# Optimization experiments

Measured on AMD Instinct MI355X. Metric: run time of the kernel, lower is better.

The kernel has to match this reference:

```python
import jax, jax.numpy as jnp
import numpy as np

N, M_CTX, SIN, YDIM, SPROJ = 16384, 4096, 256, 7, 256


def setup_inputs() -> dict:
    key = jax.random.key(0)
    k1, k2, k3, k4, k5 = jax.random.split(key, 5)
    return {
        "x": jax.random.normal(k1, (N, SIN), dtype=jnp.float32),
        "y": jax.random.normal(k2, (M_CTX, YDIM), dtype=jnp.float32),
        "Wq": jax.random.normal(k3, (SIN, SPROJ), dtype=jnp.float32) / np.sqrt(SIN),
        "Wk": jax.random.normal(k4, (YDIM, SPROJ), dtype=jnp.float32) / np.sqrt(YDIM),
        "Wv": jax.random.normal(k5, (YDIM, SPROJ), dtype=jnp.float32) / np.sqrt(YDIM),
    }


def smooth_softmax(x):
    # softmax over keys (axis=1) blended with 0.1*relu, renormalized
    s = jax.nn.softmax(x, axis=1)
    num = jax.nn.relu(x) * 0.1 + s
    return num / jnp.sum(num, axis=1, keepdims=True)


def reference(x, y, Wq, Wk, Wv):
    XQ = x @ Wq            # [N, P]
    YK = y @ Wk            # [M, P]
    YV = y @ Wv            # [M, P]
    scores = (XQ @ YK.T) / jnp.sqrt(jnp.asarray(YK.shape[1], XQ.dtype))  # [N, M]
    A = smooth_softmax(scores)
    return A @ YV          # [N, P]
```

## Files before the change

### kernel.cpp

```cpp
#include <hip/hip_runtime.h>
#include <hip/hip_bf16.h>

#define N_Q   16384
#define MCTX  4096
#define DSIN  256
#define YDIM  7
#define PDIM  256
#define BK    32
#define PSTR  40

typedef __attribute__((ext_vector_type(8))) short s16x8;
typedef __attribute__((ext_vector_type(4))) float f32x4;
typedef unsigned short u16;

static __device__ __forceinline__ u16 f2bf(float f) {
    union { float f; unsigned u; } v; v.f = f;
    unsigned r = v.u + 0x7fffu + ((v.u >> 16) & 1u);
    return (u16)(r >> 16);
}
static __device__ __forceinline__ float bf2f(u16 h) {
    union { unsigned u; float f; } v; v.u = ((unsigned)h) << 16;
    return v.f;
}
static __device__ __forceinline__ f32x4 mfma16(s16x8 a, s16x8 b, f32x4 c) {
    return __builtin_amdgcn_mfma_f32_16x16x32_bf16(a, b, c, 0, 0, 0);
}
static __device__ __forceinline__ void gload_lds16(const u16* g, u16* l) {
    __builtin_amdgcn_global_load_lds(
        (const __attribute__((address_space(1))) unsigned int*)(g),
        (__attribute__((address_space(3))) unsigned int*)(l), 16, 0, 0);
}

__global__ void k_wt(const float* __restrict__ Wq, u16* __restrict__ WtH,
                     u16* __restrict__ WtL) {
    int n = blockIdx.x;
    int k = threadIdx.x;
    float w = Wq[(size_t)k * PDIM + n];
    u16 h = f2bf(w);
    WtH[(size_t)n * DSIN + k] = h;
    WtL[(size_t)n * DSIN + k] = f2bf(w - bf2f(h));
}

__global__ void k_ykv(const float* __restrict__ y, const float* __restrict__ Wk,
                      const float* __restrict__ Wv, u16* __restrict__ YK,
                      u16* __restrict__ YVb) {
    int kb = blockIdx.x;
    int p  = threadIdx.x & 255;
    int quarter = threadIdx.x >> 8;
    float wk[YDIM], wv[YDIM];
#pragma unroll
    for (int j = 0; j < YDIM; ++j) {
        wk[j] = Wk[(size_t)j * PDIM + p];
        wv[j] = Wv[(size_t)j * PDIM + p];
    }
    s16x8 vbuf;
#pragma unroll
    for (int i = 0; i < 8; ++i) {
        int slot = quarter * 8 + i;
        int m = (slot & 1) * 16 + (slot >> 1);
        int key = kb * 32 + m;
        float ak = 0.f, av = 0.f;
#pragma unroll
        for (int j = 0; j < YDIM; ++j) {
            float yy = y[(size_t)key * YDIM + j];
            ak += yy * wk[j];
            av += yy * wv[j];
        }
        YK[(size_t)key * PDIM + p] = f2bf(ak * 0.0625f);
        vbuf[i] = (short)f2bf(av);
    }
    *(s16x8*)(YVb + ((size_t)kb * PDIM + p) * 32 + quarter * 8) = vbuf;
}

__global__ __launch_bounds__(256, 4) void k_xq(const float* __restrict__ x,
                                               const u16* __restrict__ WtH,
                                               const u16* __restrict__ WtL,
                                               u16* __restrict__ XQ) {
    __shared__ u16 xH[32 * 256];
    __shared__ u16 xL[32 * 256];
    const int tid = threadIdx.x;
    const int rowg0 = blockIdx.x * 32;

#pragma unroll
    for (int i = 0; i < 4; ++i) {
        int idx = i * 256 + tid;
        int row = idx >> 5, c32 = idx & 31;
        const float* px = x + (size_t)(rowg0 + row) * DSIN + c32 * 8;
        float4 a = *(const float4*)px;
        float4 b = *(const float4*)(px + 4);
        float vals[8] = {a.x, a.y, a.z, a.w, b.x, b.y, b.z, b.w};
        s16x8 h, l;
#pragma unroll
        for (int j = 0; j < 8; ++j) {
            u16 hh = f2bf(vals[j]);
            h[j] = (short)hh;
            l[j] = (short)f2bf(vals[j] - bf2f(hh));
        }
        int pc = c32 ^ (row & 7);
        *(s16x8*)(xH + row * 256 + pc * 8) = h;
        *(s16x8*)(xL + row * 256 + pc * 8) = l;
    }
    __syncthreads();

    const int wave = tid >> 6, lane = tid & 63;
    const int quad = lane >> 4, m16 = lane & 15;
    const int mtile = wave >> 1;
    const int phalf = (wave & 1) * 8;
    const int rowl = mtile * 16 + m16;
    const int swz = rowl & 7;
    s16x8 ah[8], al[8];
#pragma unroll
    for (int kf = 0; kf < 8; ++kf) {
        int pc = (kf * 4 + quad) ^ swz;
        ah[kf] = *(const s16x8*)(xH + rowl * 256 + pc * 8);
        al[kf] = *(const s16x8*)(xL + rowl * 256 + pc * 8);
    }
#pragma unroll
    for (int pt = 0; pt < 8; ++pt) {
        int ptg = phalf + pt;
        f32x4 acc = (f32x4){0.f, 0.f, 0.f, 0.f};
#pragma unroll
        for (int kf = 0; kf < 8; ++kf) {
            size_t idx = (size_t)(ptg * 16 + m16) * DSIN + kf * 32 + quad * 8;
            s16x8 bh = *(const s16x8*)(WtH + idx);
            s16x8 bl = *(const s16x8*)(WtL + idx);
            acc = mfma16(ah[kf], bh, acc);
            acc = mfma16(al[kf], bh, acc);
            acc = mfma16(ah[kf], bl, acc);
        }
#pragma unroll
        for (int r = 0; r < 4; ++r)
            XQ[(size_t)(rowg0 + mtile * 16 + quad * 4 + r) * PDIM + ptg * 16 + m16] =
                f2bf(acc[r]);
    }
}

__global__ __launch_bounds__(256, 2) void k_attn(const u16* __restrict__ XQ,
                                                 const u16* __restrict__ YK,
                                                 const u16* __restrict__ YVb,
                                                 u16* __restrict__ accE,
                                                 u16* __restrict__ accR,
                                                 float* __restrict__ lsum,
                                                 float* __restrict__ rsum,
                                                 int msPerSplit) {
    __shared__ u16 Kt[32 * 256];
    __shared__ u16 Pe[64 * PSTR];
    __shared__ u16 Pr[64 * PSTR];

    const int tid = threadIdx.x;
    const int wave = tid >> 6, lane = tid & 63;
    const int quad = lane >> 4, m16 = lane & 15;
    const int split = blockIdx.y;
    const int qbase = blockIdx.x * 64;
    const int key_begin = split * msPerSplit;
    const int iters = msPerSplit / BK;
    const int pslice = wave * 64;
    const int swz = m16 & 7;

    s16x8 qf[8];
    const u16* qp = XQ + (size_t)(qbase + wave * 16 + m16) * DSIN;
#pragma unroll
    for (int kf = 0; kf < 8; ++kf)
        qf[kf] = *(const s16x8*)(qp + kf * 32 + quad * 8);

    f32x4 aE[4][4], aR[4][4];
#pragma unroll
    for (int g = 0; g < 4; ++g)
#pragma unroll
        for (int t = 0; t < 4; ++t) {
            aE[g][t] = (f32x4){0.f, 0.f, 0.f, 0.f};
            aR[g][t] = (f32x4){0.f, 0.f, 0.f, 0.f};
        }
    float lacc[4] = {0.f, 0.f, 0.f, 0.f}, racc[4] = {0.f, 0.f, 0.f, 0.f};

    auto stage = [&](int key0) {
#pragma unroll
        for (int c = 0; c < 4; ++c) {
            int l = (wave * 4 + c) * 64 + lane;
            int r = l >> 5;
            int sc = (l & 31) ^ (r & 7);
            gload_lds16(YK + (size_t)(key0 + r) * DSIN + sc * 8,
                        Kt + (size_t)(wave * 4 + c) * 512);
        }
    };
    stage(key_begin);

    for (int it = 0; it < iters; ++it) {
        const int key0 = key_begin + it * BK;
        __syncthreads();

        f32x4 s0 = (f32x4){0.f, 0.f, 0.f, 0.f};
        f32x4 s1 = (f32x4){0.f, 0.f, 0.f, 0.f};
#pragma unroll
        for (int kf = 0; kf < 8; ++kf) {
            int pc = (kf * 4 + quad) ^ swz;
            s16x8 b0 = *(const s16x8*)(Kt + m16 * 256 + pc * 8);
            s16x8 b1 = *(const s16x8*)(Kt + (16 + m16) * 256 + pc * 8);
            s0 = mfma16(qf[kf], b0, s0);
            s1 = mfma16(qf[kf], b1, s1);
        }
#pragma unroll
        for (int r = 0; r < 4; ++r) {
            float e0 = __expf(s0[r]), e1 = __expf(s1[r]);
            float rl0 = fmaxf(s0[r], 0.f), rl1 = fmaxf(s1[r], 0.f);
            lacc[r] += e0 + e1;
            racc[r] += rl0 + rl1;
            int row = wave * 16 + quad * 4 + r;
            unsigned pe = (unsigned)f2bf(e0) | ((unsigned)f2bf(e1) << 16);
            unsigned pr = (unsigned)f2bf(rl0) | ((unsigned)f2bf(rl1) << 16);
            *(unsigned*)(&Pe[row * PSTR + 2 * m16]) = pe;
            *(unsigned*)(&Pr[row * PSTR + 2 * m16]) = pr;
        }
        __syncthreads();

        s16x8 vf[4];
        const u16* vb = YVb + (size_t)((key0 >> 5) * PDIM) * 32;
#pragma unroll
        for (int t = 0; t < 4; ++t)
            vf[t] = *(const s16x8*)(vb + (size_t)(pslice + t * 16 + m16) * 32 + quad * 8);

        if (it + 1 < iters) stage(key0 + BK);

#pragma unroll
        for (int g = 0; g < 4; ++g) {
            s16x8 pa = *(const s16x8*)(&Pe[(g * 16 + m16) * PSTR + quad * 8]);
            s16x8 pb = *(const s16x8*)(&Pr[(g * 16 + m16) * PSTR + quad * 8]);
#pragma unroll
            for (int t = 0; t < 4; ++t) {
                aE[g][t] = mfma16(pa, vf[t], aE[g][t]);
                aR[g][t] = mfma16(pb, vf[t], aR[g][t]);
            }
        }
    }

    size_t ob = ((size_t)split * N_Q + qbase) * PDIM;
#pragma unroll
    for (int g = 0; g < 4; ++g)
#pragma unroll
        for (int t = 0; t < 4; ++t)
#pragma unroll
            for (int r = 0; r < 4; ++r) {
                size_t o = ob + (size_t)(g * 16 + quad * 4 + r) * PDIM + pslice + t * 16 + m16;
                accE[o] = f2bf(aE[g][t][r]);
                accR[o] = f2bf(aR[g][t][r]);
            }
#pragma unroll
    for (int r = 0; r < 4; ++r) {
        lacc[r] += __shfl_xor(lacc[r], 1);
        lacc[r] += __shfl_xor(lacc[r], 2);
        lacc[r] += __shfl_xor(lacc[r], 4);
        lacc[r] += __shfl_xor(lacc[r], 8);
        racc[r] += __shfl_xor(racc[r], 1);
        racc[r] += __shfl_xor(racc[r], 2);
        racc[r] += __shfl_xor(racc[r], 4);
        racc[r] += __shfl_xor(racc[r], 8);
    }
    if (m16 < 4) {
        float lv = (m16 == 0) ? lacc[0] : (m16 == 1) ? lacc[1] : (m16 == 2) ? lacc[2] : lacc[3];
        float rv = (m16 == 0) ? racc[0] : (m16 == 1) ? racc[1] : (m16 == 2) ? racc[2] : racc[3];
        int row = split * N_Q + qbase + wave * 16 + quad * 4 + m16;
        lsum[row] = lv;
        rsum[row] = rv;
    }
}

__global__ void k_comb(const u16* __restrict__ accE, const u16* __restrict__ accR,
                       const float* __restrict__ lsum, const float* __restrict__ rsum,
                       float* __restrict__ out, int nsplit) {
    size_t chunk = (size_t)blockIdx.x * 256 + threadIdx.x;
    int row = (int)(chunk >> 5);
    size_t base = (size_t)row * PDIM + (chunk & 31) * 8;
    const size_t NP = (size_t)N_Q * PDIM;
    float E[8], R[8];
#pragma unroll
    for (int j = 0; j < 8; ++j) { E[j] = 0.f; R[j] = 0.f; }
    float L = 0.f, Rs = 0.f;
    for (int s = 0; s < nsplit; ++s) {
        s16x8 e = *(const s16x8*)(accE + s * NP + base);
        s16x8 r = *(const s16x8*)(accR + s * NP + base);
#pragma unroll
        for (int j = 0; j < 8; ++j) {
            E[j] += bf2f((u16)e[j]);
            R[j] += bf2f((u16)r[j]);
        }
        L  += lsum[(size_t)s * N_Q + row];
        Rs += rsum[(size_t)s * N_Q + row];
    }
    float invL = 1.f / L, invD = 1.f / (1.f + 0.1f * Rs);
    float4 o0, o1;
    o0.x = (0.1f * R[0] + E[0] * invL) * invD;
    o0.y = (0.1f * R[1] + E[1] * invL) * invD;
    o0.z = (0.1f * R[2] + E[2] * invL) * invD;
    o0.w = (0.1f * R[3] + E[3] * invL) * invD;
    o1.x = (0.1f * R[4] + E[4] * invL) * invD;
    o1.y = (0.1f * R[5] + E[5] * invL) * invD;
    o1.z = (0.1f * R[6] + E[6] * invL) * invD;
    o1.w = (0.1f * R[7] + E[7] * invL) * invD;
    *(float4*)(out + base) = o0;
    *(float4*)(out + base + 4) = o1;
}

extern "C" void kernel_launch(void* const* d_in, const int* in_sizes, int n_in,
                              void* d_out, int out_size, void* d_ws, size_t ws_size,
                              hipStream_t stream) {
    const float* x  = (const float*)d_in[0];
    const float* y  = (const float*)d_in[1];
    const float* Wq = (const float*)d_in[2];
    const float* Wk = (const float*)d_in[3];
    const float* Wv = (const float*)d_in[4];
    float* out = (float*)d_out;

    char* ws = (char*)d_ws;
    size_t off = 0;
    auto take = [&](size_t bytes) -> char* {
        char* p = ws + off;
        off += (bytes + 255) & ~(size_t)255;
        return p;
    };
    u16* XQ  = (u16*)take((size_t)N_Q * PDIM * 2);
    u16* WtH = (u16*)take((size_t)PDIM * DSIN * 2);
    u16* WtL = (u16*)take((size_t)PDIM * DSIN * 2);
    u16* YK  = (u16*)take((size_t)MCTX * PDIM * 2);
    u16* YVb = (u16*)take((size_t)MCTX * PDIM * 2);

    size_t perSplit = (size_t)N_Q * PDIM * 2 * 2 + (size_t)N_Q * 4 * 2 + 1024;
    int nsplit = 1;
    if (ws_size >= off + 4 * perSplit + 4096) nsplit = 4;
    else if (ws_size >= off + 2 * perSplit + 4096) nsplit = 2;

    u16*   accE = (u16*)take((size_t)nsplit * N_Q * PDIM * 2);
    u16*   accR = (u16*)take((size_t)nsplit * N_Q * PDIM * 2);
    float* lsum = (float*)take((size_t)nsplit * N_Q * 4);
    float* rsum = (float*)take((size_t)nsplit * N_Q * 4);

    hipLaunchKernelGGL(k_wt,   dim3(PDIM),     dim3(DSIN), 0, stream, Wq, WtH, WtL);
    hipLaunchKernelGGL(k_ykv,  dim3(MCTX/32),  dim3(1024), 0, stream, y, Wk, Wv, YK, YVb);
    hipLaunchKernelGGL(k_xq,   dim3(N_Q/32),   dim3(256),  0, stream, x, WtH, WtL, XQ);
    hipLaunchKernelGGL(k_attn, dim3(N_Q/64, nsplit), dim3(256), 0, stream,
                       XQ, YK, YVb, accE, accR, lsum, rsum, MCTX / nsplit);
    hipLaunchKernelGGL(k_comb, dim3((N_Q * PDIM) / (256 * 8)), dim3(256), 0, stream,
                       accE, accR, lsum, rsum, out, nsplit);
}
```

Baseline: 239.6 us.

## Switch attention matmuls to FP8 MFMA with split-precision queries

Moves the score and PV matmuls from bf16 to fp8 MFMA. K, V and the probability tiles are stored as fp8, and the query is split into hi/lo fp8 parts to keep score accuracy. This halves LDS and global traffic for K/V/P and uses the higher-rate fp8 path, at the cost of doubling the score MFMAs and adding scaling and clamping (exp capped at 440 to stay in fp8 range), which risks accuracy. It also stores XQ in fp32 and caps the key split at 2.

Result: no change. 239.2 us (-0.2%).

```diff
diff --git a/kernel.cpp b/kernel.cpp
--- a/kernel.cpp
+++ b/kernel.cpp
@@ -7,11 +7,14 @@
 #define YDIM  7
 #define PDIM  256
 #define BK    32
-#define PSTR  40
+#define PSTRB 40
 
 typedef __attribute__((ext_vector_type(8))) short s16x8;
 typedef __attribute__((ext_vector_type(4))) float f32x4;
 typedef unsigned short u16;
+typedef unsigned char  u8;
+typedef long long      i64;
+typedef unsigned long long u64;
 
 static __device__ __forceinline__ u16 f2bf(float f) {
     union { float f; unsigned u; } v; v.f = f;
@@ -22,10 +25,30 @@
     union { unsigned u; float f; } v; v.u = ((unsigned)h) << 16;
     return v.f;
 }
-static __device__ __forceinline__ f32x4 mfma16(s16x8 a, s16x8 b, f32x4 c) {
+static __device__ __forceinline__ f32x4 mfma_bf16(s16x8 a, s16x8 b, f32x4 c) {
     return __builtin_amdgcn_mfma_f32_16x16x32_bf16(a, b, c, 0, 0, 0);
 }
-static __device__ __forceinline__ void gload_lds16(const u16* g, u16* l) {
+static __device__ __forceinline__ f32x4 mfma_fp8(i64 a, i64 b, f32x4 c) {
+    return __builtin_amdgcn_mfma_f32_16x16x32_fp8_fp8(a, b, c, 0, 0, 0);
+}
+static __device__ __forceinline__ unsigned cvt2fp8(float a, float b) {
+    return (unsigned)__builtin_amdgcn_cvt_pk_fp8_f32(a, b, 0, false) & 0xffffu;
+}
+static __device__ __forceinline__ i64 pack_fp8x8(const float* v) {
+    unsigned w0 = (unsigned)__builtin_amdgcn_cvt_pk_fp8_f32(v[0], v[1], 0, false);
+    w0 = (unsigned)__builtin_amdgcn_cvt_pk_fp8_f32(v[2], v[3], (int)w0, true);
+    unsigned w1 = (unsigned)__builtin_amdgcn_cvt_pk_fp8_f32(v[4], v[5], 0, false);
+    w1 = (unsigned)__builtin_amdgcn_cvt_pk_fp8_f32(v[6], v[7], (int)w1, true);
+    return (i64)(((u64)w1 << 32) | w0);
+}
+static __device__ __forceinline__ float fp8dec(unsigned b) {
+    unsigned s = b >> 7, e = (b >> 3) & 15, m = b & 7;
+    if (e == 0) return (s ? -1.f : 1.f) * (float)m * 0.001953125f;
+    union { unsigned u; float f; } v;
+    v.u = (s << 31) | ((e + 120u) << 23) | (m << 20);
+    return v.f;
+}
+static __device__ __forceinline__ void gload_lds16(const void* g, void* l) {
     __builtin_amdgcn_global_load_lds(
         (const __attribute__((address_space(1))) unsigned int*)(g),
         (__attribute__((address_space(3))) unsigned int*)(l), 16, 0, 0);
@@ -42,8 +65,8 @@
 }
 
 __global__ void k_ykv(const float* __restrict__ y, const float* __restrict__ Wk,
-                      const float* __restrict__ Wv, u16* __restrict__ YK,
-                      u16* __restrict__ YVb) {
+                      const float* __restrict__ Wv, u8* __restrict__ YK8,
+                      u8* __restrict__ YVb8) {
     int kb = blockIdx.x;
     int p  = threadIdx.x & 255;
     int quarter = threadIdx.x >> 8;
@@ -53,7 +76,7 @@
         wk[j] = Wk[(size_t)j * PDIM + p];
         wv[j] = Wv[(size_t)j * PDIM + p];
     }
-    s16x8 vbuf;
+    float vv[8];
 #pragma unroll
     for (int i = 0; i < 8; ++i) {
         int slot = quarter * 8 + i;
@@ -66,16 +89,16 @@
             ak += yy * wk[j];
             av += yy * wv[j];
         }
-        YK[(size_t)key * PDIM + p] = f2bf(ak * 0.0625f);
-        vbuf[i] = (short)f2bf(av);
-    }
-    *(s16x8*)(YVb + ((size_t)kb * PDIM + p) * 32 + quarter * 8) = vbuf;
+        YK8[(size_t)key * PDIM + p] = (u8)(cvt2fp8(ak * 0.25f, 0.f) & 0xff);
+        vv[i] = av;
+    }
+    *(i64*)(YVb8 + ((size_t)kb * PDIM + p) * 32 + quarter * 8) = pack_fp8x8(vv);
 }
 
 __global__ __launch_bounds__(256, 4) void k_xq(const float* __restrict__ x,
                                                const u16* __restrict__ WtH,
                                                const u16* __restrict__ WtL,
-                                               u16* __restrict__ XQ) {
+                                               float* __restrict__ XQ) {
     __shared__ u16 xH[32 * 256];
     __shared__ u16 xL[32 * 256];
     const int tid = threadIdx.x;
@@ -124,28 +147,28 @@
             size_t idx = (size_t)(ptg * 16 + m16) * DSIN + kf * 32 + quad * 8;
             s16x8 bh = *(const s16x8*)(WtH + idx);
             s16x8 bl = *(const s16x8*)(WtL + idx);
-            acc = mfma16(ah[kf], bh, acc);
-            acc = mfma16(al[kf], bh, acc);
-            acc = mfma16(ah[kf], bl, acc);
+            acc = mfma_bf16(ah[kf], bh, acc);
+            acc = mfma_bf16(al[kf], bh, acc);
+            acc = mfma_bf16(ah[kf], bl, acc);
         }
 #pragma unroll
         for (int r = 0; r < 4; ++r)
             XQ[(size_t)(rowg0 + mtile * 16 + quad * 4 + r) * PDIM + ptg * 16 + m16] =
-                f2bf(acc[r]);
-    }
-}
-
-__global__ __launch_bounds__(256, 2) void k_attn(const u16* __restrict__ XQ,
-                                                 const u16* __restrict__ YK,
-                                                 const u16* __restrict__ YVb,
+                acc[r];
+    }
+}
+
+__global__ __launch_bounds__(256, 2) void k_attn(const float* __restrict__ XQ,
+                                                 const u8* __restrict__ YK8,
+                                                 const u8* __restrict__ YVb8,
                                                  u16* __restrict__ accE,
                                                  u16* __restrict__ accR,
                                                  float* __restrict__ lsum,
                                                  float* __restrict__ rsum,
                                                  int msPerSplit) {
-    __shared__ u16 Kt[32 * 256];
-    __shared__ u16 Pe[64 * PSTR];
-    __shared__ u16 Pr[64 * PSTR];
+    __shared__ u8 Kt[32 * 256];
+    __shared__ u8 Pe[64 * PSTRB];
+    __shared__ u8 Pr[64 * PSTRB];
 
     const int tid = threadIdx.x;
     const int wave = tid >> 6, lane = tid & 63;
@@ -155,13 +178,27 @@
     const int key_begin = split * msPerSplit;
     const int iters = msPerSplit / BK;
     const int pslice = wave * 64;
-    const int swz = m16 & 7;
-
-    s16x8 qf[8];
-    const u16* qp = XQ + (size_t)(qbase + wave * 16 + m16) * DSIN;
-#pragma unroll
-    for (int kf = 0; kf < 8; ++kf)
-        qf[kf] = *(const s16x8*)(qp + kf * 32 + quad * 8);
+
+    i64 qhi[8], qlo[8];
+    {
+        const float* qp = XQ + (size_t)(qbase + wave * 16 + m16) * PDIM;
+#pragma unroll
+        for (int kf = 0; kf < 8; ++kf) {
+            const float4* q4 = (const float4*)(qp + kf * 32 + quad * 8);
+            float4 a = q4[0], b = q4[1];
+            float qv[8] = {a.x * 0.25f, a.y * 0.25f, a.z * 0.25f, a.w * 0.25f,
+                           b.x * 0.25f, b.y * 0.25f, b.z * 0.25f, b.w * 0.25f};
+            i64 hi = pack_fp8x8(qv);
+            float lv[8];
+#pragma unroll
+            for (int j = 0; j < 8; ++j) {
+                unsigned hb = (unsigned)(((u64)hi >> (8 * j)) & 0xff);
+                lv[j] = (qv[j] - fp8dec(hb)) * 16.0f;
+            }
+            qhi[kf] = hi;
+            qlo[kf] = pack_fp8x8(lv);
+        }
+    }
 
     f32x4 aE[4][4], aR[4][4];
 #pragma unroll
@@ -175,12 +212,12 @@
 
     auto stage = [&](int key0) {
 #pragma unroll
-        for (int c = 0; c < 4; ++c) {
-            int l = (wave * 4 + c) * 64 + lane;
-            int r = l >> 5;
-            int sc = (l & 31) ^ (r & 7);
-            gload_lds16(YK + (size_t)(key0 + r) * DSIN + sc * 8,
-                        Kt + (size_t)(wave * 4 + c) * 512);
+        for (int c = 0; c < 2; ++c) {
+            int l = (wave * 2 + c) * 64 + lane;
+            int r = l >> 4;
+            int sc = (l & 15) ^ (r & 15);
+            gload_lds16(YK8 + (size_t)(key0 + r) * PDIM + sc * 16,
+                        Kt + (size_t)(wave * 2 + c) * 1024);
         }
     };
     stage(key_begin);
@@ -189,46 +226,51 @@
         const int key0 = key_begin + it * BK;
         __syncthreads();
 
-        f32x4 s0 = (f32x4){0.f, 0.f, 0.f, 0.f};
-        f32x4 s1 = (f32x4){0.f, 0.f, 0.f, 0.f};
+        f32x4 s0h = (f32x4){0.f, 0.f, 0.f, 0.f};
+        f32x4 s1h = (f32x4){0.f, 0.f, 0.f, 0.f};
+        f32x4 s0l = (f32x4){0.f, 0.f, 0.f, 0.f};
+        f32x4 s1l = (f32x4){0.f, 0.f, 0.f, 0.f};
 #pragma unroll
         for (int kf = 0; kf < 8; ++kf) {
-            int pc = (kf * 4 + quad) ^ swz;
-            s16x8 b0 = *(const s16x8*)(Kt + m16 * 256 + pc * 8);
-            s16x8 b1 = *(const s16x8*)(Kt + (16 + m16) * 256 + pc * 8);
-            s0 = mfma16(qf[kf], b0, s0);
-            s1 = mfma16(qf[kf], b1, s1);
+            int gp = (((kf * 4 + quad) ^ (2 * m16)) & 31) * 8;
+            i64 b0 = *(const i64*)(Kt + m16 * 256 + gp);
+            i64 b1 = *(const i64*)(Kt + (16 + m16) * 256 + gp);
+            s0h = mfma_fp8(qhi[kf], b0, s0h);
+            s1h = mfma_fp8(qhi[kf], b1, s1h);
+            s0l = mfma_fp8(qlo[kf], b0, s0l);
+            s1l = mfma_fp8(qlo[kf], b1, s1l);
         }
 #pragma unroll
         for (int r = 0; r < 4; ++r) {
-            float e0 = __expf(s0[r]), e1 = __expf(s1[r]);
-            float rl0 = fmaxf(s0[r], 0.f), rl1 = fmaxf(s1[r], 0.f);
+            float sv0 = s0h[r] + 0.0625f * s0l[r];
+            float sv1 = s1h[r] + 0.0625f * s1l[r];
+            float e0 = fminf(__expf(sv0), 440.f);
+            float e1 = fminf(__expf(sv1), 440.f);
+            float rl0 = fmaxf(sv0, 0.f), rl1 = fmaxf(sv1, 0.f);
             lacc[r] += e0 + e1;
             racc[r] += rl0 + rl1;
             int row = wave * 16 + quad * 4 + r;
-            unsigned pe = (unsigned)f2bf(e0) | ((unsigned)f2bf(e1) << 16);
-            unsigned pr = (unsigned)f2bf(rl0) | ((unsigned)f2bf(rl1) << 16);
-            *(unsigned*)(&Pe[row * PSTR + 2 * m16]) = pe;
-            *(unsigned*)(&Pr[row * PSTR + 2 * m16]) = pr;
+            *(u16*)(Pe + row * PSTRB + 2 * m16) = (u16)cvt2fp8(e0, e1);
+            *(u16*)(Pr + row * PSTRB + 2 * m16) = (u16)cvt2fp8(rl0, rl1);
         }
         __syncthreads();
 
-        s16x8 vf[4];
-        const u16* vb = YVb + (size_t)((key0 >> 5) * PDIM) * 32;
+        i64 vf[4];
+        const u8* vb = YVb8 + (size_t)(key0 >> 5) * PDIM * 32;
 #pragma unroll
         for (int t = 0; t < 4; ++t)
-            vf[t] = *(const s16x8*)(vb + (size_t)(pslice + t * 16 + m16) * 32 + quad * 8);
+            vf[t] = *(const i64*)(vb + (size_t)(pslice + t * 16 + m16) * 32 + quad * 8);
 
         if (it + 1 < iters) stage(key0 + BK);
 
 #pragma unroll
         for (int g = 0; g < 4; ++g) {
-            s16x8 pa = *(const s16x8*)(&Pe[(g * 16 + m16) * PSTR + quad * 8]);
-            s16x8 pb = *(const s16x8*)(&Pr[(g * 16 + m16) * PSTR + quad * 8]);
+            i64 pa = *(const i64*)(Pe + (g * 16 + m16) * PSTRB + quad * 8);
+            i64 pb = *(const i64*)(Pr + (g * 16 + m16) * PSTRB + quad * 8);
 #pragma unroll
             for (int t = 0; t < 4; ++t) {
-                aE[g][t] = mfma16(pa, vf[t], aE[g][t]);
-                aR[g][t] = mfma16(pb, vf[t], aR[g][t]);
+                aE[g][t] = mfma_fp8(pa, vf[t], aE[g][t]);
+                aR[g][t] = mfma_fp8(pb, vf[t], aR[g][t]);
             }
         }
     }
@@ -317,16 +359,14 @@
         off += (bytes + 255) & ~(size_t)255;
         return p;
     };
-    u16* XQ  = (u16*)take((size_t)N_Q * PDIM * 2);
-    u16* WtH = (u16*)take((size_t)PDIM * DSIN * 2);
-    u16* WtL = (u16*)take((size_t)PDIM * DSIN * 2);
-    u16* YK  = (u16*)take((size_t)MCTX * PDIM * 2);
-    u16* YVb = (u16*)take((size_t)MCTX * PDIM * 2);
+    float* XQ  = (float*)take((size_t)N_Q * PDIM * 4);
+    u16* WtH   = (u16*)take((size_t)PDIM * DSIN * 2);
+    u16* WtL   = (u16*)take((size_t)PDIM * DSIN * 2);
+    u8*  YK8   = (u8*)take((size_t)MCTX * PDIM);
+    u8*  YVb8  = (u8*)take((size_t)MCTX * PDIM);
 
     size_t perSplit = (size_t)N_Q * PDIM * 2 * 2 + (size_t)N_Q * 4 * 2 + 1024;
-    int nsplit = 1;
-    if (ws_size >= off + 4 * perSplit + 4096) nsplit = 4;
-    else if (ws_size >= off + 2 * perSplit + 4096) nsplit = 2;
+    int nsplit = (ws_size >= off + 2 * perSplit + 4096) ? 2 : 1;
 
     u16*   accE = (u16*)take((size_t)nsplit * N_Q * PDIM * 2);
     u16*   accR = (u16*)take((size_t)nsplit * N_Q * PDIM * 2);
@@ -334,10 +374,10 @@
     float* rsum = (float*)take((size_t)nsplit * N_Q * 4);
 
     hipLaunchKernelGGL(k_wt,   dim3(PDIM),     dim3(DSIN), 0, stream, Wq, WtH, WtL);
-    hipLaunchKernelGGL(k_ykv,  dim3(MCTX/32),  dim3(1024), 0, stream, y, Wk, Wv, YK, YVb);
+    hipLaunchKernelGGL(k_ykv,  dim3(MCTX/32),  dim3(1024), 0, stream, y, Wk, Wv, YK8, YVb8);
     hipLaunchKernelGGL(k_xq,   dim3(N_Q/32),   dim3(256),  0, stream, x, WtH, WtL, XQ);
     hipLaunchKernelGGL(k_attn, dim3(N_Q/64, nsplit), dim3(256), 0, stream,
-                       XQ, YK, YVb, accE, accR, lsum, rsum, MCTX / nsplit);
+                       XQ, YK8, YVb8, accE, accR, lsum, rsum, MCTX / nsplit);
     hipLaunchKernelGGL(k_comb, dim3((N_Q * PDIM) / (256 * 8)), dim3(256), 0, stream,
                        accE, accR, lsum, rsum, out, nsplit);
 }
```
